# Kernel optimization log

Hardware: AMD Instinct MI355X
Metric: run time of the kernel (lower is better)

The kernel has to match this reference:

```python
import jax, jax.numpy as jnp
import numpy as np

D_IN, D_H, D_G, H, B = 512, 256, 128, 8, 4096
EPS_LN = 1e-6
EPS_STD = 1e-6


def setup_inputs() -> dict:
    key = jax.random.key(0)
    ks = jax.random.split(key, 4)
    x = jax.random.normal(ks[0], (B, D_IN), dtype=jnp.float32)
    # Dense params (flax kernel layout: (in, out)), lecun-normal-ish init
    Wh = jax.random.normal(ks[1], (D_IN, D_H), dtype=jnp.float32) / np.sqrt(D_IN)
    bh = jnp.zeros((D_H,), dtype=jnp.float32)
    Wz1 = jax.random.normal(ks[2], (D_IN, H * D_H), dtype=jnp.float32) / np.sqrt(D_IN)
    Wz2 = jax.random.normal(ks[3], (D_IN, H * D_G), dtype=jnp.float32) / np.sqrt(D_IN)
    ln_scale = jnp.ones((D_H,), dtype=jnp.float32)
    ln_bias = jnp.zeros((D_H,), dtype=jnp.float32)
    return {"x": x, "Wh": Wh, "bh": bh, "Wz1": Wz1, "Wz2": Wz2,
            "ln_scale": ln_scale, "ln_bias": ln_bias}


def _layer_norm(a, scale, bias):
    mu = jnp.mean(a, axis=-1, keepdims=True)
    var = jnp.var(a, axis=-1, keepdims=True)
    return (a - mu) * jax.lax.rsqrt(var + EPS_LN) * scale + bias


def reference(x, Wh, bh, Wz1, Wz2, ln_scale, ln_bias):
    sz_b = x.shape[0]
    # h: (B, d_h)
    h = _layer_norm(jax.nn.relu(x @ Wh + bh), ln_scale, ln_bias)
    z1 = (x @ Wz1).reshape(sz_b, H, D_H)   # (B, H, d_h)
    z2 = (x @ Wz2).reshape(sz_b, H, D_G)   # (B, H, d_g)
    # w = z2^T @ z1 over heads: (B, d_g, d_h)
    w = jnp.einsum('bhg,bhd->bgd', z2, z1)
    # per-row standardization (population std, ddof=0) + tanh
    mu = jnp.mean(w, axis=-1, keepdims=True)
    sd = jnp.std(w, axis=-1, keepdims=True)
    w = jnp.tanh((w - mu) / (sd + EPS_STD))
    # y = w @ h: (B, d_g)
    y = jnp.einsum('bgd,bd->bg', w, h)
    return h, y
```

## Files before the change

kernel.cpp:

```cpp
#include <hip/hip_runtime.h>
#include <hip/hip_bf16.h>
#include <cstdint>

#define BATCH 4096
#define DIN   512
#define DH    256
#define DG    128
#define NH    8
#define NTOT  3328
#define RPB   2
#define SH    264
#define RREG  (9 * SH)

typedef __bf16 bf16x8 __attribute__((ext_vector_type(8)));
typedef float  f32x4  __attribute__((ext_vector_type(4)));

__device__ __forceinline__ unsigned short f2bf(float f) {
    union { float f; uint32_t u; } v; v.f = f;
    uint32_t u = v.u;
    u += 0x7fffu + ((u >> 16) & 1u);
    return (unsigned short)(u >> 16);
}
__device__ __forceinline__ float bf2f(unsigned short s) {
    union { uint32_t u; float f; } v; v.u = ((uint32_t)s) << 16;
    return v.f;
}

__device__ __forceinline__ void async16(const unsigned short* g, unsigned short* l) {
    __builtin_amdgcn_global_load_lds(
        (const __attribute__((address_space(1))) unsigned int*)(uintptr_t)g,
        (__attribute__((address_space(3))) unsigned int*)(uintptr_t)l,
        16, 0, 0);
}

__global__ __launch_bounds__(256) void prep_kernel(const float* __restrict__ x,
                                                   const float* __restrict__ Wh,
                                                   const float* __restrict__ Wz1,
                                                   const float* __restrict__ Wz2,
                                                   unsigned short* __restrict__ xb,
                                                   unsigned short* __restrict__ Wt) {
    __shared__ float tile[32][33];
    int bid = blockIdx.x;
    int t = threadIdx.x;
    if (bid < 2048) {
        int i = (bid * 256 + t) * 4;
        float4 v = *(const float4*)(x + i);
        ushort4 o;
        o.x = f2bf(v.x); o.y = f2bf(v.y); o.z = f2bf(v.z); o.w = f2bf(v.w);
        *(ushort4*)(xb + i) = o;
        return;
    }
    int b2 = bid - 2048;
    int n0 = (b2 % 104) * 32;
    int k0 = (b2 / 104) * 32;
    const float* W; int ldn, nl;
    if (n0 < 256)       { W = Wh;  ldn = 256;  nl = n0; }
    else if (n0 < 2304) { W = Wz1; ldn = 2048; nl = n0 - 256; }
    else                { W = Wz2; ldn = 1024; nl = n0 - 2304; }
    int tx = t & 31, ty = t >> 5;
    #pragma unroll
    for (int i = 0; i < 4; i++) {
        int kk = ty + i * 8;
        tile[kk][tx] = W[(size_t)(k0 + kk) * ldn + nl + tx];
    }
    __syncthreads();
    #pragma unroll
    for (int i = 0; i < 4; i++) {
        int nn = ty + i * 8;
        Wt[(size_t)(n0 + nn) * 512 + k0 + tx] = f2bf(tile[tx][nn]);
    }
}

__global__ __launch_bounds__(256) void gemm_kernel(const unsigned short* __restrict__ xb,
                                                   const unsigned short* __restrict__ Wt,
                                                   unsigned short* __restrict__ Zb) {
    __shared__ unsigned short As[128 * 32];
    __shared__ unsigned short Bs[128 * 32];
    const int m0 = blockIdx.y * 128;
    const int n0 = blockIdx.x * 128;
    const int t = threadIdx.x;
    const int w = t >> 6, lane = t & 63;
    const int wm = (w >> 1) * 64, wn = (w & 1) * 64;
    const int lrow = lane & 15, q = lane >> 4;
    const int swz = q ^ (lrow & 3);

    f32x4 acc[4][4] = {};

    for (int k0 = 0; k0 < DIN; k0 += 32) {
        __syncthreads();
        #pragma unroll
        for (int j = 0; j < 2; j++) {
            int gidx = (w * 2 + j) * 64 + lane;
            int row = gidx >> 2, slot = gidx & 3;
            int src = slot ^ (row & 3);
            const unsigned short* ga = xb + (size_t)(m0 + row) * DIN + k0 + src * 8;
            const unsigned short* gb = Wt + (size_t)(n0 + row) * DIN + k0 + src * 8;
            async16(ga, As + (w * 2 + j) * 512);
            async16(gb, Bs + (w * 2 + j) * 512);
        }
        __syncthreads();
        bf16x8 af[4], bfr[4];
        #pragma unroll
        for (int i = 0; i < 4; i++) {
            int row = wm + i * 16 + lrow;
            af[i] = *reinterpret_cast<const bf16x8*>(As + row * 32 + ((q ^ (row & 3)) * 8));
        }
        #pragma unroll
        for (int j = 0; j < 4; j++) {
            int row = wn + j * 16 + lrow;
            bfr[j] = *reinterpret_cast<const bf16x8*>(Bs + row * 32 + ((q ^ (row & 3)) * 8));
        }
        #pragma unroll
        for (int i = 0; i < 4; i++)
            #pragma unroll
            for (int j = 0; j < 4; j++)
                acc[i][j] = __builtin_amdgcn_mfma_f32_16x16x32_bf16(af[i], bfr[j], acc[i][j], 0, 0, 0);
    }
    #pragma unroll
    for (int i = 0; i < 4; i++)
        #pragma unroll
        for (int j = 0; j < 4; j++) {
            int col = n0 + wn + j * 16 + lrow;
            int rbase = m0 + wm + i * 16 + q * 4;
            #pragma unroll
            for (int r = 0; r < 4; r++)
                Zb[(size_t)(rbase + r) * NTOT + col] = f2bf(acc[i][j][r]);
        }
}

__global__ __launch_bounds__(256, 4) void attn_kernel(const unsigned short* __restrict__ Zb,
                                                      const float* __restrict__ bh,
                                                      const float* __restrict__ lns,
                                                      const float* __restrict__ lnb,
                                                      float* __restrict__ h_out,
                                                      float* __restrict__ y_out) {
    __shared__ __align__(16) unsigned short z1a[RPB * RREG + 7 * SH];
    __shared__ __align__(16) unsigned short z1cb[RPB][DH * 8];
    __shared__ __align__(16) unsigned short z2b[RPB][1024];
    __shared__ __align__(16) unsigned short z2A[RPB][1024];
    __shared__ __align__(16) float hsr[RPB][DH];
    __shared__ float GLr[RPB][9][9];
    __shared__ float redH[RPB];
    __shared__ __align__(16) unsigned short zpad[8];
    const int b0 = blockIdx.x * RPB;
    const int t = threadIdx.x;
    const int wv = t >> 6, lane = t & 63;
    const int lrow = lane & 15, q = lane >> 4;

    #pragma unroll
    for (int r = 0; r < RPB; r++) {
        uint4 v = *(const uint4*)(Zb + (size_t)(b0 + r) * NTOT + 256 + t * 8);
        *(uint4*)(z1a + r * RREG + (t >> 5) * SH + (t & 31) * 8) = v;
        z1a[r * RREG + 8 * SH + t] = 0x3F80;
    }
    {
        int r = t >> 7, c = t & 127;
        uint4 v = *(const uint4*)(Zb + (size_t)(b0 + r) * NTOT + 2304 + c * 8);
        *(uint4*)(&z2b[r][c * 8]) = v;
    }
    if (t < 8) zpad[t] = 0;
    __syncthreads();

    if (wv < 2) {
        int r = wv, d0 = lane * 4;
        const unsigned short* Zr = Zb + (size_t)(b0 + r) * NTOT;
        ushort4 hu = *(const ushort4*)(Zr + d0);
        float4 bv = *(const float4*)(bh + d0);
        float vv[4];
        vv[0] = fmaxf(bf2f(hu.x) + bv.x, 0.f);
        vv[1] = fmaxf(bf2f(hu.y) + bv.y, 0.f);
        vv[2] = fmaxf(bf2f(hu.z) + bv.z, 0.f);
        vv[3] = fmaxf(bf2f(hu.w) + bv.w, 0.f);
        float s = vv[0] + vv[1] + vv[2] + vv[3];
        float sq = vv[0] * vv[0] + vv[1] * vv[1] + vv[2] * vv[2] + vv[3] * vv[3];
        #pragma unroll
        for (int m = 32; m >= 1; m >>= 1) {
            s  += __shfl_xor(s,  m, 64);
            sq += __shfl_xor(sq, m, 64);
        }
        float mu  = s * (1.0f / 256.0f);
        float var = sq * (1.0f / 256.0f) - mu * mu;
        float rs = rsqrtf(var + 1e-6f);
        float4 lv = *(const float4*)(lns + d0);
        float4 ov = *(const float4*)(lnb + d0);
        float hv0 = (vv[0] - mu) * rs * lv.x + ov.x;
        float hv1 = (vv[1] - mu) * rs * lv.y + ov.y;
        float hv2 = (vv[2] - mu) * rs * lv.z + ov.z;
        float hv3 = (vv[3] - mu) * rs * lv.w + ov.w;
        *(float4*)(&hsr[r][d0]) = float4{hv0, hv1, hv2, hv3};
        *(float4*)(h_out + (size_t)(b0 + r) * DH + d0) = float4{hv0, hv1, hv2, hv3};
        float hp = hv0 + hv1 + hv2 + hv3;
        #pragma unroll
        for (int m = 32; m >= 1; m >>= 1) hp += __shfl_xor(hp, m, 64);
        if (lane == 0) redH[r] = hp;
    } else {
        int r = wv - 2;
        f32x4 g = {};
        #pragma unroll
        for (int ks = 0; ks < 8; ks++) {
            bf16x8 fr = *reinterpret_cast<const bf16x8*>(z1a + r * RREG + lrow * SH + ks * 32 + q * 8);
            g = __builtin_amdgcn_mfma_f32_16x16x32_bf16(fr, fr, g, 0, 0, 0);
        }
        #pragma unroll
        for (int i = 0; i < 4; i++) {
            int crow = q * 4 + i;
            if (crow < 9 && lrow < 9) GLr[r][crow][lrow] = g[i];
        }
    }
    __syncthreads();

    const int sr = t >> 7, sg = t & 127;
    {
        float mh[NH];
        #pragma unroll
        for (int h = 0; h < NH; h++) mh[h] = GLr[sr][h][8] * (1.0f / 256.0f);
        #pragma unroll
        for (int it = 0; it < 2; it++) {
            int d = sg + it * 128;
            uint32_t pk[4];
            #pragma unroll
            for (int h2 = 0; h2 < 4; h2++) {
                float c0 = bf2f(z1a[sr * RREG + (2 * h2) * SH + d])     - mh[2 * h2];
                float c1 = bf2f(z1a[sr * RREG + (2 * h2 + 1) * SH + d]) - mh[2 * h2 + 1];
                pk[h2] = (uint32_t)f2bf(c0) | ((uint32_t)f2bf(c1) << 16);
            }
            *(uint4*)(&z1cb[sr][d * 8]) = uint4{pk[0], pk[1], pk[2], pk[3]};
        }
    }
    {
        float z2g[NH];
        #pragma unroll
        for (int h = 0; h < NH; h++) z2g[h] = bf2f(z2b[sr][h * 128 + sg]);
        float mug = 0.f, qg = 0.f;
        #pragma unroll
        for (int h = 0; h < NH; h++) {
            mug += z2g[h] * GLr[sr][h][8];
            float inn = 0.f;
            #pragma unroll
            for (int h2 = 0; h2 < NH; h2++) inn += z2g[h2] * GLr[sr][h][h2];
            qg += z2g[h] * inn;
        }
        mug *= (1.0f / 256.0f);
        qg  *= (1.0f / 256.0f);
        float vg = fmaxf(qg - mug * mug, 0.0f);
        float A = 2.0f * 1.4426950408889634f / (sqrtf(vg) + 1e-6f);
        uint32_t pk[4];
        #pragma unroll
        for (int h2 = 0; h2 < 4; h2++)
            pk[h2] = (uint32_t)f2bf(z2g[2 * h2] * A) | ((uint32_t)f2bf(z2g[2 * h2 + 1] * A) << 16);
        *(uint4*)(&z2A[sr][sg * 8]) = uint4{pk[0], pk[1], pk[2], pk[3]};
    }
    __syncthreads();

    const int row = wv >> 1, gtb = (wv & 1) * 4;
    const unsigned short* bp = (q == 0) ? (&z1cb[row][lrow * 8]) : zpad;
    const int binc = (q == 0) ? 128 : 0;
    bf16x8 af[4];
    #pragma unroll
    for (int gt = 0; gt < 4; gt++) {
        const unsigned short* pa = (q == 0) ? (&z2A[row][((gtb + gt) * 16 + lrow) * 8]) : zpad;
        af[gt] = *reinterpret_cast<const bf16x8*>(pa);
    }
    f32x4 czero = {};
    float yn[4][4] = {};
    #pragma unroll 4
    for (int dt = 0; dt < 16; dt++) {
        bf16x8 bfr = *reinterpret_cast<const bf16x8*>(bp + dt * binc);
        float hv = hsr[row][dt * 16 + lrow];
        #pragma unroll
        for (int gt = 0; gt < 4; gt++) {
            f32x4 c = __builtin_amdgcn_mfma_f32_16x16x32_bf16(af[gt], bfr, czero, 0, 0, 0);
            #pragma unroll
            for (int r4 = 0; r4 < 4; r4++) {
                float e = __builtin_amdgcn_exp2f(c[r4]);
                yn[gt][r4] = fmaf(hv, __builtin_amdgcn_rcpf(e + 1.0f), yn[gt][r4]);
            }
        }
    }
    #pragma unroll
    for (int m = 1; m <= 8; m <<= 1)
        #pragma unroll
        for (int gt = 0; gt < 4; gt++)
            #pragma unroll
            for (int r4 = 0; r4 < 4; r4++)
                yn[gt][r4] += __shfl_xor(yn[gt][r4], m, 64);
    if (lrow == 0) {
        float Hs = redH[row];
        #pragma unroll
        for (int gt = 0; gt < 4; gt++)
            #pragma unroll
            for (int r4 = 0; r4 < 4; r4++)
                y_out[(size_t)(b0 + row) * DG + (gtb + gt) * 16 + q * 4 + r4] = Hs - 2.0f * yn[gt][r4];
    }
}

extern "C" void kernel_launch(void* const* d_in, const int* in_sizes, int n_in,
                              void* d_out, int out_size, void* d_ws, size_t ws_size,
                              hipStream_t stream) {
    const float* x   = (const float*)d_in[0];
    const float* Wh  = (const float*)d_in[1];
    const float* bh  = (const float*)d_in[2];
    const float* Wz1 = (const float*)d_in[3];
    const float* Wz2 = (const float*)d_in[4];
    const float* lns = (const float*)d_in[5];
    const float* lnb = (const float*)d_in[6];
    float* h_out = (float*)d_out;
    float* y_out = h_out + (size_t)BATCH * DH;

    char* ws = (char*)d_ws;
    unsigned short* Zb = (unsigned short*)ws;
    unsigned short* xb = (unsigned short*)(ws + 27262976);
    unsigned short* Wt = (unsigned short*)(ws + 31457280);

    prep_kernel<<<3712, 256, 0, stream>>>(x, Wh, Wz1, Wz2, xb, Wt);
    gemm_kernel<<<dim3(NTOT / 128, BATCH / 128), 256, 0, stream>>>(xb, Wt, Zb);
    attn_kernel<<<BATCH / RPB, 256, 0, stream>>>(Zb, bh, lns, lnb, h_out, y_out);
}
```

Measured before the change: 140.5 us.

## Rewrite GEMM as 256x256 tile with double-buffered LDS pipelining

Replaces the 128x128, 256-thread GEMM with a 256x256 tile computed by 8 waves, K-step 64. Shared memory is double-buffered, and the next K-tile is staged asynchronously in quarters interleaved with the MFMA phases, with explicit vmcnt waits, barriers and setprio. This is meant to hide global-load latency and raise arithmetic intensity per block. The cost is 128KB of LDS per block and only 13x16 = 208 blocks, so occupancy and wave count drop and tail effects may appear.

```diff
diff --git a/kernel.cpp b/kernel.cpp
--- a/kernel.cpp
+++ b/kernel.cpp
@@ -71,53 +71,106 @@
     }
 }
 
-__global__ __launch_bounds__(256) void gemm_kernel(const unsigned short* __restrict__ xb,
-                                                   const unsigned short* __restrict__ Wt,
-                                                   unsigned short* __restrict__ Zb) {
-    __shared__ unsigned short As[128 * 32];
-    __shared__ unsigned short Bs[128 * 32];
-    const int m0 = blockIdx.y * 128;
-    const int n0 = blockIdx.x * 128;
+__device__ __forceinline__ void stage_half(const unsigned short* g, unsigned short* l,
+                                           int ktn, int rl, int lch, int wv) {
+    async16(g + (size_t)rl * 512 + ktn * 64 + lch * 8,        l + wv * 512);
+    async16(g + (size_t)(rl + 64) * 512 + ktn * 64 + lch * 8, l + 4096 + wv * 512);
+}
+
+__global__ __launch_bounds__(512, 2) void gemm_kernel(const unsigned short* __restrict__ xb,
+                                                      const unsigned short* __restrict__ Wt,
+                                                      unsigned short* __restrict__ Zb) {
+    __shared__ unsigned short As[2][256 * 64];
+    __shared__ unsigned short Bs[2][256 * 64];
+    const int m0 = blockIdx.y * 256;
+    const int n0 = blockIdx.x * 256;
     const int t = threadIdx.x;
-    const int w = t >> 6, lane = t & 63;
-    const int wm = (w >> 1) * 64, wn = (w & 1) * 64;
+    const int wv = t >> 6, lane = t & 63;
     const int lrow = lane & 15, q = lane >> 4;
-    const int swz = q ^ (lrow & 3);
-
-    f32x4 acc[4][4] = {};
-
-    for (int k0 = 0; k0 < DIN; k0 += 32) {
-        __syncthreads();
-        #pragma unroll
-        for (int j = 0; j < 2; j++) {
-            int gidx = (w * 2 + j) * 64 + lane;
-            int row = gidx >> 2, slot = gidx & 3;
-            int src = slot ^ (row & 3);
-            const unsigned short* ga = xb + (size_t)(m0 + row) * DIN + k0 + src * 8;
-            const unsigned short* gb = Wt + (size_t)(n0 + row) * DIN + k0 + src * 8;
-            async16(ga, As + (w * 2 + j) * 512);
-            async16(gb, Bs + (w * 2 + j) * 512);
-        }
-        __syncthreads();
-        bf16x8 af[4], bfr[4];
-        #pragma unroll
-        for (int i = 0; i < 4; i++) {
-            int row = wm + i * 16 + lrow;
-            af[i] = *reinterpret_cast<const bf16x8*>(As + row * 32 + ((q ^ (row & 3)) * 8));
-        }
-        #pragma unroll
-        for (int j = 0; j < 4; j++) {
-            int row = wn + j * 16 + lrow;
-            bfr[j] = *reinterpret_cast<const bf16x8*>(Bs + row * 32 + ((q ^ (row & 3)) * 8));
-        }
-        #pragma unroll
-        for (int i = 0; i < 4; i++)
-            #pragma unroll
-            for (int j = 0; j < 4; j++)
-                acc[i][j] = __builtin_amdgcn_mfma_f32_16x16x32_bf16(af[i], bfr[j], acc[i][j], 0, 0, 0);
-    }
-    #pragma unroll
-    for (int i = 0; i < 4; i++)
+    const int wm = (wv >> 2) * 128;
+    const int wn = (wv & 3) * 64;
+
+    const int rl  = wv * 8 + (lane >> 3);
+    const int lch = ((lane & 7) - (lane >> 3)) & 7;
+    const int sw0 = ((q + (lrow & 7)) & 7) * 8;
+    const int sw1 = ((4 + q + (lrow & 7)) & 7) * 8;
+
+    const unsigned short* gA = xb + (size_t)m0 * 512;
+    const unsigned short* gB = Wt + (size_t)n0 * 512;
+
+    f32x4 acc[8][4] = {};
+
+#define MFMA16(MH) \
+    _Pragma("unroll") for (int f = 0; f < 4; f++) \
+      _Pragma("unroll") for (int n = 0; n < 4; n++) \
+        acc[(MH) * 4 + f][n] = __builtin_amdgcn_mfma_f32_16x16x32_bf16(af[f], bfv[n], acc[(MH) * 4 + f][n], 0, 0, 0)
+
+#define FRAG_READS(MH, SW) \
+    bf16x8 af[4], bfv[4]; \
+    _Pragma("unroll") for (int f = 0; f < 4; f++) \
+        af[f] = *reinterpret_cast<const bf16x8*>(Ab + (wm + (MH) * 64 + f * 16 + lrow) * 64 + (SW)); \
+    _Pragma("unroll") for (int n = 0; n < 4; n++) \
+        bfv[n] = *reinterpret_cast<const bf16x8*>(Bb + (wn + n * 16 + lrow) * 64 + (SW))
+
+    stage_half(gA,             &As[0][0],    0, rl, lch, wv);
+    stage_half(gA + 128 * 512, &As[0][8192], 0, rl, lch, wv);
+    stage_half(gB,             &Bs[0][0],    0, rl, lch, wv);
+    stage_half(gB + 128 * 512, &Bs[0][8192], 0, rl, lch, wv);
+
+    #pragma unroll 1
+    for (int kt = 0; kt < 8; ++kt) {
+        const int cur = kt & 1, nxt = cur ^ 1;
+        const int ktn = (kt + 1) & 7;
+        const unsigned short* Ab = &As[cur][0];
+        const unsigned short* Bb = &Bs[cur][0];
+        unsigned short* An = &As[nxt][0];
+        unsigned short* Bn = &Bs[nxt][0];
+
+        stage_half(gA, An, ktn, rl, lch, wv);
+        asm volatile("s_waitcnt vmcnt(2)" ::: "memory");
+        __builtin_amdgcn_s_barrier();
+        {
+            FRAG_READS(0, sw0);
+            __builtin_amdgcn_s_setprio(1);
+            MFMA16(0);
+            __builtin_amdgcn_s_setprio(0);
+            __builtin_amdgcn_s_barrier();
+        }
+        {
+            FRAG_READS(0, sw1);
+            stage_half(gA + 128 * 512, An + 8192, ktn, rl, lch, wv);
+            __builtin_amdgcn_s_barrier();
+            __builtin_amdgcn_s_setprio(1);
+            MFMA16(0);
+            __builtin_amdgcn_s_setprio(0);
+            __builtin_amdgcn_s_barrier();
+        }
+        {
+            FRAG_READS(1, sw0);
+            stage_half(gB, Bn, ktn, rl, lch, wv);
+            __builtin_amdgcn_s_barrier();
+            __builtin_amdgcn_s_setprio(1);
+            MFMA16(1);
+            __builtin_amdgcn_s_setprio(0);
+            __builtin_amdgcn_s_barrier();
+        }
+        {
+            FRAG_READS(1, sw1);
+            stage_half(gB + 128 * 512, Bn + 8192, ktn, rl, lch, wv);
+            __builtin_amdgcn_s_barrier();
+            __builtin_amdgcn_s_setprio(1);
+            MFMA16(1);
+            __builtin_amdgcn_s_setprio(0);
+            __builtin_amdgcn_s_barrier();
+        }
+    }
+    asm volatile("s_waitcnt vmcnt(0)" ::: "memory");
+
+#undef FRAG_READS
+#undef MFMA16
+
+    #pragma unroll
+    for (int i = 0; i < 8; i++)
         #pragma unroll
         for (int j = 0; j < 4; j++) {
             int col = n0 + wn + j * 16 + lrow;
@@ -313,6 +366,6 @@
     unsigned short* Wt = (unsigned short*)(ws + 31457280);
 
     prep_kernel<<<3712, 256, 0, stream>>>(x, Wh, Wz1, Wz2, xb, Wt);
-    gemm_kernel<<<dim3(NTOT / 128, BATCH / 128), 256, 0, stream>>>(xb, Wt, Zb);
+    gemm_kernel<<<dim3(NTOT / 256, BATCH / 256), 512, 0, stream>>>(xb, Wt, Zb);
     attn_kernel<<<BATCH / RPB, 256, 0, stream>>>(Zb, bh, lns, lnb, h_out, y_out);
 }
```

Result: faster. 132.1 us (median of 3 runs) (-6.0%).
